# Performance work log

Hardware: AMD Instinct MI355X
Metric: run time of the kernel (lower is better)

## Reference

```python
import jax, jax.numpy as jnp
import numpy as np

H = 256       # hidden_dim
D = 64        # dim_dynamic
T = 49        # pooler_resolution**2 tokens
B = 4800      # N * nr_boxes
NP = H * D    # num_params
NOUT = H * T  # flattened output features
EPS = 1e-5


def _ln(x, g, b):
    mu = jnp.mean(x, axis=-1, keepdims=True)
    var = jnp.mean(jnp.square(x - mu), axis=-1, keepdims=True)
    return (x - mu) * jax.lax.rsqrt(var + EPS) * g + b


def setup_inputs() -> dict:
    key = jax.random.key(0)
    ks = jax.random.split(key, 12)
    s = 0.02
    inp = {
        "pro_features": jax.random.normal(ks[0], (1, B, H), jnp.float32),
        "roi_features": jax.random.normal(ks[1], (T, B, H), jnp.float32),
        # dynamic_layer: Linear(H, 2*H*D)
        "dyn_w": jax.random.normal(ks[2], (2 * NP, H), jnp.float32) * s,
        "dyn_b": jnp.zeros((2 * NP,), jnp.float32),
        "n1_g": jnp.ones((D,), jnp.float32), "n1_b": jnp.zeros((D,), jnp.float32),
        "n2_g": jnp.ones((H,), jnp.float32), "n2_b": jnp.zeros((H,), jnp.float32),
        # proj_cls1/2: Linear(H, H//8), Linear(H//8, H)
        "pc1_w": jax.random.normal(ks[3], (H // 8, H), jnp.float32) * s,
        "pc1_b": jnp.zeros((H // 8,), jnp.float32),
        "pc2_w": jax.random.normal(ks[4], (H, H // 8), jnp.float32) * s,
        "pc2_b": jnp.zeros((H,), jnp.float32),
        "n3c_g": jnp.ones((H,), jnp.float32), "n3c_b": jnp.zeros((H,), jnp.float32),
        "pr1_w": jax.random.normal(ks[5], (H // 8, H), jnp.float32) * s,
        "pr1_b": jnp.zeros((H // 8,), jnp.float32),
        "pr2_w": jax.random.normal(ks[6], (H, H // 8), jnp.float32) * s,
        "pr2_b": jnp.zeros((H,), jnp.float32),
        "n3r_g": jnp.ones((H,), jnp.float32), "n3r_b": jnp.zeros((H,), jnp.float32),
        # out_layer_cls/reg: Linear(H*T, H)
        "oc_w": jax.random.normal(ks[7], (H, NOUT), jnp.float32) * s,
        "oc_b": jnp.zeros((H,), jnp.float32),
        "n4c_g": jnp.ones((H,), jnp.float32), "n4c_b": jnp.zeros((H,), jnp.float32),
        "or_w": jax.random.normal(ks[8], (H, NOUT), jnp.float32) * s,
        "or_b": jnp.zeros((H,), jnp.float32),
        "n4r_g": jnp.ones((H,), jnp.float32), "n4r_b": jnp.zeros((H,), jnp.float32),
    }
    return inp


def reference(pro_features, roi_features, dyn_w, dyn_b, n1_g, n1_b, n2_g, n2_b,
              pc1_w, pc1_b, pc2_w, pc2_b, n3c_g, n3c_b,
              pr1_w, pr1_b, pr2_w, pr2_b, n3r_g, n3r_b,
              oc_w, oc_b, n4c_g, n4c_b, or_w, or_b, n4r_g, n4r_b):
    pro = pro_features[0]                      # (B, H)
    feats = roi_features.transpose(1, 0, 2)    # (B, T, H)
    params = pro @ dyn_w.T + dyn_b             # (B, 2*H*D)
    p1 = params[:, :NP].reshape(-1, H, D)      # (B, H, D)
    p2 = params[:, NP:].reshape(-1, D, H)      # (B, D, H)
    x = jnp.einsum('bth,bhd->btd', feats, p1)  # (B, T, D)
    x = jax.nn.relu(_ln(x, n1_g, n1_b))
    x = jnp.einsum('btd,bdh->bth', x, p2)      # (B, T, H)
    x = jax.nn.relu(_ln(x, n2_g, n2_b))
    mask_cls = jax.nn.sigmoid((pro @ pc1_w.T + pc1_b) @ pc2_w.T + pc2_b)  # (B, H)
    mask_reg = jax.nn.sigmoid((pro @ pr1_w.T + pr1_b) @ pr2_w.T + pr2_b)  # (B, H)
    fc = jax.nn.relu(_ln(x * mask_cls[:, None, :], n3c_g, n3c_b))  # (B, T, H)
    fr = jax.nn.relu(_ln(x * mask_reg[:, None, :], n3r_g, n3r_b))  # (B, T, H)
    fc = fc.reshape(fc.shape[0], -1) @ oc_w.T + oc_b               # (B, H)
    fc = jax.nn.relu(_ln(fc, n4c_g, n4c_b))
    fr = fr.reshape(fr.shape[0], -1) @ or_w.T + or_b               # (B, H)
    fr = jax.nn.relu(_ln(fr, n4r_g, n4r_b))
    return (fc, fr)
```

## Files before the change

kernel.cpp:

```cpp
#include <hip/hip_runtime.h>

#define Hc 256
#define Dc 64
#define Tc 49
#define Bc 4800
#define NPc 16384
#define KOUT 12544
#define OUTSTRIDE 1228800

typedef unsigned short u16;
typedef unsigned int u32;
typedef __bf16 bf16x8 __attribute__((ext_vector_type(8)));
typedef float f32x4 __attribute__((ext_vector_type(4)));

__device__ __forceinline__ u16 f2bf(float f){
  u32 u = __builtin_bit_cast(u32, f);
  u += 0x7fffu + ((u >> 16) & 1u);
  return (u16)(u >> 16);
}

#define GLDS16(gp, lp) __builtin_amdgcn_global_load_lds((const __attribute__((address_space(1))) void*)(gp), (__attribute__((address_space(3))) void*)(lp), 16, 0, 0)

__device__ __forceinline__ f32x4 mfma16(bf16x8 a, bf16x8 b, f32x4 c){
  return __builtin_amdgcn_mfma_f32_16x16x32_bf16(a, b, c, 0, 0, 0);
}
__device__ __forceinline__ f32x4 zero4(){ f32x4 v; v[0]=0.f; v[1]=0.f; v[2]=0.f; v[3]=0.f; return v; }

__global__ void cvt_kernel(const float* __restrict__ src, u16* __restrict__ dst, int n){
  int i = (blockIdx.x*256 + threadIdx.x)*4;
  if (i >= n) return;
  float4 v = *(const float4*)(src + i);
  u16 t[4] = {f2bf(v.x), f2bf(v.y), f2bf(v.z), f2bf(v.w)};
  *(uint2*)(dst + i) = *(const uint2*)t;
}

__global__ void procvt_kernel(const float* __restrict__ src, u16* __restrict__ dst){
  int i = (blockIdx.x*256 + threadIdx.x)*4;
  u16 t[4];
  if (i < Bc*Hc){
    float4 v = *(const float4*)(src + i);
    t[0]=f2bf(v.x); t[1]=f2bf(v.y); t[2]=f2bf(v.z); t[3]=f2bf(v.w);
  } else { t[0]=t[1]=t[2]=t[3]=0; }
  *(uint2*)(dst + i) = *(const uint2*)t;
}

__device__ __forceinline__ int dynperm(int n){
  if (n < NPc){
    int h = n >> 6, d = n & 63;
    return (d>>4)*4096 + (h>>5)*512 + ((h>>3)&3)*128 + (d&15)*8 + (h&7);
  } else {
    int m = n - NPc; int d = m >> 8, h = m & 255;
    return NPc + (h>>4)*1024 + (d>>5)*512 + ((d>>3)&3)*128 + (h&15)*8 + (d&7);
  }
}

__global__ __launch_bounds__(256) void cvt_dynw_perm(const float* __restrict__ dynw,
    const float* __restrict__ dynb, u16* __restrict__ dynwB, float* __restrict__ dynbP){
  int idx = blockIdx.x*256 + threadIdx.x;
  int n = idx >> 3, p = idx & 7;
  int pn = dynperm(n);
  const float* s = dynw + (size_t)n*256 + p*32;
  u16 t[32];
  #pragma unroll
  for (int j = 0; j < 8; j++){
    float4 v = *(const float4*)(s + j*4);
    t[j*4+0]=f2bf(v.x); t[j*4+1]=f2bf(v.y); t[j*4+2]=f2bf(v.z); t[j*4+3]=f2bf(v.w);
  }
  u16* d = dynwB + (size_t)pn*256 + p*32;
  #pragma unroll
  for (int j = 0; j < 4; j++) ((uint4*)d)[j] = ((const uint4*)t)[j];
  if (p == 0) dynbP[pn] = dynb[n];
}

__global__ __launch_bounds__(256) void masks_kernel(const float* __restrict__ pro,
    const float* __restrict__ pc1w, const float* __restrict__ pc1b,
    const float* __restrict__ pc2w, const float* __restrict__ pc2b,
    const float* __restrict__ pr1w, const float* __restrict__ pr1b,
    const float* __restrict__ pr2w, const float* __restrict__ pr2b,
    float* __restrict__ mcls, float* __restrict__ mreg)
{
  __shared__ float rowv[8][256];
  __shared__ float hv[8][33];
  const int tid = threadIdx.x;
  const int bb = blockIdx.x*8;
  #pragma unroll
  for (int q = 0; q < 8; q++) rowv[q][tid] = pro[(size_t)(bb+q)*256 + tid];
  const int bx = tid >> 5, h = tid & 31;
  __syncthreads();
  for (int br = 0; br < 2; br++){
    const float* w1 = br ? pr1w : pc1w;
    const float* b1 = br ? pr1b : pc1b;
    const float* w2 = br ? pr2w : pc2w;
    const float* b2 = br ? pr2b : pc2b;
    float* outm = br ? mreg : mcls;
    {
      float s = b1[h];
      const float* wr = w1 + h*256;
      for (int k = 0; k < 256; k += 4){
        float4 wv = *(const float4*)(wr + k);
        s += rowv[bx][k]*wv.x + rowv[bx][k+1]*wv.y + rowv[bx][k+2]*wv.z + rowv[bx][k+3]*wv.w;
      }
      hv[bx][h] = s;
    }
    __syncthreads();
    int c0 = h*8;
    float o[8];
    #pragma unroll
    for (int j = 0; j < 8; j++){
      float s2 = b2[c0+j];
      const float* w2r = w2 + (c0+j)*32;
      #pragma unroll
      for (int j2 = 0; j2 < 32; j2 += 4){
        float4 wv = *(const float4*)(w2r + j2);
        s2 += hv[bx][j2]*wv.x + hv[bx][j2+1]*wv.y + hv[bx][j2+2]*wv.z + hv[bx][j2+3]*wv.w;
      }
      o[j] = 1.f/(1.f + expf(-s2));
    }
    float* dst = outm + (size_t)(bb+bx)*256 + c0;
    *(float4*)dst = make_float4(o[0],o[1],o[2],o[3]);
    *(float4*)(dst+4) = make_float4(o[4],o[5],o[6],o[7]);
    __syncthreads();
  }
}

__global__ __launch_bounds__(512, 4) void gemm1_kernel(const u16* __restrict__ proB,
    const u16* __restrict__ dynwB, const float* __restrict__ dynbP,
    u16* __restrict__ paramsOut, int b0, int C)
{
  __shared__ u16 sm[2][2][128*64];
  const int tid = threadIdx.x;
  const int bx = blockIdx.x, by = blockIdx.y;
  const int l = tid & 63, wid = tid >> 6, l15 = l & 15, lg = l >> 4;
  const int wm = wid >> 2, wn = wid & 3;
  const char* Abase = (const char*)proB;
  const char* Bbase = (const char*)dynwB;

  auto stage = [&](int t, int buf){
    #pragma unroll
    for (int p = 0; p < 2; p++){
      int base = (wid + p*8)*1024;
      int lin = base + l*16;
      int row = lin >> 7, cb = lin & 127;
      int swz = (row & 7) << 4;
      GLDS16(Abase + (size_t)(b0 + bx*128 + row)*512 + t*128 + (cb ^ swz),
             (char*)sm[buf][0] + base);
      GLDS16(Bbase + (size_t)(by*128 + row)*512 + t*128 + (cb ^ swz),
             (char*)sm[buf][1] + base);
    }
  };

  f32x4 acc[4][2];
  #pragma unroll
  for (int i=0;i<4;i++){ acc[i][0]=zero4(); acc[i][1]=zero4(); }

  stage(0, 0);
  __syncthreads();
  for (int t = 0; t < 4; t++){
    if (t < 3) stage(t+1, (t&1)^1);
    const char* sa = (const char*)sm[t&1][0];
    const char* sb = (const char*)sm[t&1][1];
    #pragma unroll
    for (int ks = 0; ks < 2; ks++){
      bf16x8 av[4], bv[2];
      #pragma unroll
      for (int mt=0; mt<4; mt++){
        int row = wm*64 + mt*16 + l15;
        av[mt] = *(const bf16x8*)(sa + row*128 + ((ks*64 + lg*16) ^ ((row&7)<<4)));
      }
      #pragma unroll
      for (int nt=0; nt<2; nt++){
        int row = wn*32 + nt*16 + l15;
        bv[nt] = *(const bf16x8*)(sb + row*128 + ((ks*64 + lg*16) ^ ((row&7)<<4)));
      }
      #pragma unroll
      for (int mt=0; mt<4; mt++)
        #pragma unroll
        for (int nt=0; nt<2; nt++)
          acc[mt][nt] = mfma16(av[mt], bv[nt], acc[mt][nt]);
    }
    __syncthreads();
  }
  float bb[2];
  #pragma unroll
  for (int nt=0; nt<2; nt++) bb[nt] = dynbP[by*128 + wn*32 + nt*16 + l15];
  char* tile = (char*)sm;
  #pragma unroll
  for (int mt=0; mt<4; mt++)
    #pragma unroll
    for (int nt=0; nt<2; nt++)
      #pragma unroll
      for (int r=0; r<4; r++){
        int row = wm*64 + mt*16 + lg*4 + r;
        int col = wn*32 + nt*16 + l15;
        *(u16*)(tile + row*256 + ((col*2) ^ ((row&7)<<4))) = f2bf(acc[mt][nt][r] + bb[nt]);
      }
  __syncthreads();
  #pragma unroll
  for (int p = 0; p < 4; p++){
    int lin = (tid + p*512)*16;
    int row = lin >> 8, cb = lin & 255;
    int rg = bx*128 + row;
    if (rg < C){
      uint4 v = *(const uint4*)(tile + row*256 + (cb ^ ((row&7)<<4)));
      *(uint4*)((char*)paramsOut + (size_t)rg*65536 + (size_t)by*256 + cb) = v;
    }
  }
}

__global__ __launch_bounds__(256, 3) void conv_kernel(const float* __restrict__ roi,
    const u16* __restrict__ params,
    const float* __restrict__ n1g, const float* __restrict__ n1b,
    const float* __restrict__ n2g, const float* __restrict__ n2b,
    const float* __restrict__ n3cg, const float* __restrict__ n3cb,
    const float* __restrict__ n3rg, const float* __restrict__ n3rb,
    const float* __restrict__ mcls, const float* __restrict__ mreg,
    u16* __restrict__ fcin, u16* __restrict__ frin, int b0)
{
  __shared__ char lds[49152];
  const int tid = threadIdx.x, bloc = blockIdx.x, b = b0 + bloc;
  const int l = tid & 63, w = tid >> 6, l15 = l & 15, lg = l >> 4;
  const char* pbase = (const char*)params + (size_t)bloc*65536;
  const int myrow = 16*w + l15;
  const int rrow = tid >> 2, rk4 = tid & 3;
  const float* rsrc = roi + ((size_t)rrow*Bc + b)*256 + rk4*32;

  float4 rva[8];
  if (rrow < Tc){
    #pragma unroll
    for (int j = 0; j < 8; j++) rva[j] = *(const float4*)(rsrc + j*4);
  }
  #pragma unroll
  for (int p = 0; p < 4; p++)
    GLDS16(pbase + p*8192 + tid*16, lds + 16384 + p*4096 + w*1024);

  float* SCf = (float*)(lds + 40960);
  {
    float mc = mcls[(size_t)b*256+tid], mr = mreg[(size_t)b*256+tid];
    float g2 = n2g[tid], b2v = n2b[tid];
    SCf[0*256+tid] = g2*mc; SCf[1*256+tid] = b2v*mc;
    SCf[2*256+tid] = n3cg[tid]; SCf[3*256+tid] = n3cb[tid];
    SCf[4*256+tid] = g2*mr; SCf[5*256+tid] = b2v*mr;
    SCf[6*256+tid] = n3rg[tid]; SCf[7*256+tid] = n3rb[tid];
  }

  auto wfeats = [&](const float4* rv){
    u16 tt[32];
    if (rrow < Tc){
      #pragma unroll
      for (int j = 0; j < 8; j++){
        float4 v = rv[j];
        tt[j*4+0]=f2bf(v.x); tt[j*4+1]=f2bf(v.y); tt[j*4+2]=f2bf(v.z); tt[j*4+3]=f2bf(v.w);
      }
    } else {
      #pragma unroll
      for (int j=0;j<32;j++) tt[j]=0;
    }
    int swz = (rrow & 7) << 4;
    #pragma unroll
    for (int c2 = 0; c2 < 4; c2++)
      *(uint4*)(lds + rrow*256 + ((rk4*64 + c2*16) ^ swz)) = ((const uint4*)tt)[c2];
  };
  wfeats(rva);
  float4 rvb[8];
  if (rrow < Tc){
    #pragma unroll
    for (int j = 0; j < 8; j++) rvb[j] = *(const float4*)(rsrc + 128 + j*4);
  }
  __syncthreads();

  f32x4 xacc[4];
  #pragma unroll
  for (int i=0;i<4;i++) xacc[i] = zero4();
  #pragma unroll
  for (int ks = 0; ks < 4; ks++){
    bf16x8 af = *(const bf16x8*)(lds + myrow*256 + ((ks*64 + lg*16) ^ ((myrow&7)<<4)));
    #pragma unroll
    for (int nt = 0; nt < 4; nt++){
      bf16x8 bf = *(const bf16x8*)(lds + 16384 + nt*4096 + ks*1024 + lg*256 + l15*16);
      xacc[nt] = mfma16(af, bf, xacc[nt]);
    }
  }
  __syncthreads();
  #pragma unroll
  for (int p = 0; p < 4; p++)
    GLDS16(pbase + p*8192 + 4096 + tid*16, lds + 16384 + p*4096 + w*1024);
  wfeats(rvb);
  __syncthreads();
  #pragma unroll
  for (int ks = 0; ks < 4; ks++){
    bf16x8 af = *(const bf16x8*)(lds + myrow*256 + ((ks*64 + lg*16) ^ ((myrow&7)<<4)));
    #pragma unroll
    for (int nt = 0; nt < 4; nt++){
      bf16x8 bf = *(const bf16x8*)(lds + 16384 + nt*4096 + ks*1024 + lg*256 + l15*16);
      xacc[nt] = mfma16(af, bf, xacc[nt]);
    }
  }
  __syncthreads();

  #pragma unroll
  for (int p = 0; p < 8; p++)
    GLDS16(pbase + 32768 + p*4096 + tid*16, lds + p*4096 + w*1024);
  {
    float g1v[4], b1v[4];
    #pragma unroll
    for (int nt=0; nt<4; nt++){ g1v[nt] = n1g[nt*16+l15]; b1v[nt] = n1b[nt*16+l15]; }
    #pragma unroll
    for (int r = 0; r < 4; r++){
      float s = xacc[0][r]+xacc[1][r]+xacc[2][r]+xacc[3][r];
      float q = xacc[0][r]*xacc[0][r]+xacc[1][r]*xacc[1][r]
              + xacc[2][r]*xacc[2][r]+xacc[3][r]*xacc[3][r];
      #pragma unroll
      for (int m = 1; m < 16; m <<= 1){ s += __shfl_xor(s, m); q += __shfl_xor(q, m); }
      float mu = s*(1.f/64.f);
      float rs = rsqrtf(q*(1.f/64.f) - mu*mu + 1e-5f);
      int row = 16*w + lg*4 + r;
      int swz = (row & 7) << 4;
      #pragma unroll
      for (int nt=0; nt<4; nt++){
        float yv = fmaxf((xacc[nt][r]-mu)*rs*g1v[nt] + b1v[nt], 0.f);
        *(u16*)(lds + 32768 + row*128 + ((2*(nt*16+l15)) ^ swz)) = f2bf(yv);
      }
    }
  }
  __syncthreads();

  f32x4 acc[16];
  #pragma unroll
  for (int i=0;i<16;i++) acc[i] = zero4();
  #pragma unroll
  for (int ks = 0; ks < 2; ks++){
    bf16x8 ay = *(const bf16x8*)(lds + 32768 + myrow*128 + ((ks*64 + lg*16) ^ ((myrow&7)<<4)));
    #pragma unroll
    for (int nt = 0; nt < 16; nt++){
      bf16x8 bp = *(const bf16x8*)(lds + nt*2048 + ks*1024 + lg*256 + l15*16);
      acc[nt] = mfma16(ay, bp, acc[nt]);
    }
  }

  #pragma unroll
  for (int r = 0; r < 4; r++){
    float s = 0.f, q = 0.f;
    #pragma unroll
    for (int nt=0; nt<16; nt++){ float v = acc[nt][r]; s += v; q += v*v; }
    #pragma unroll
    for (int m = 1; m < 16; m <<= 1){ s += __shfl_xor(s, m); q += __shfl_xor(q, m); }
    float mu = s*(1.f/256.f);
    float rs = rsqrtf(q*(1.f/256.f) - mu*mu + 1e-5f);
    #pragma unroll
    for (int nt=0; nt<16; nt++) acc[nt][r] = (acc[nt][r]-mu)*rs;
  }
  __syncthreads();

  float* SCf2 = (float*)(lds + 40960);
  for (int br = 0; br < 2; br++){
    float s3[4] = {0.f,0.f,0.f,0.f}, q3[4] = {0.f,0.f,0.f,0.f};
    #pragma unroll
    for (int nt=0; nt<16; nt++){
      int col = nt*16 + l15;
      float gm = SCf2[(4*br)*256 + col], bm = SCf2[(4*br+1)*256 + col];
      #pragma unroll
      for (int r=0; r<4; r++){
        float u = fmaxf(acc[nt][r]*gm + bm, 0.f);
        s3[r] += u; q3[r] += u*u;
      }
    }
    float m3[4], r3[4];
    #pragma unroll
    for (int r=0; r<4; r++){
      float s = s3[r], q = q3[r];
      #pragma unroll
      for (int m = 1; m < 16; m <<= 1){ s += __shfl_xor(s, m); q += __shfl_xor(q, m); }
      float mu = s*(1.f/256.f);
      m3[r] = mu; r3[r] = rsqrtf(q*(1.f/256.f) - mu*mu + 1e-5f);
    }
    #pragma unroll
    for (int nt=0; nt<16; nt++){
      int col = nt*16 + l15;
      float gm = SCf2[(4*br)*256 + col], bm = SCf2[(4*br+1)*256 + col];
      float g3 = SCf2[(4*br+2)*256 + col], b3 = SCf2[(4*br+3)*256 + col];
      #pragma unroll
      for (int r=0; r<4; r++){
        int row = 16*w + lg*4 + r;
        float u = fmaxf(acc[nt][r]*gm + bm, 0.f);
        float f = fmaxf((u - m3[r])*r3[r]*g3 + b3, 0.f);
        *(u16*)(lds + row*512 + ((2*col) ^ ((row&7)<<4))) = f2bf(f);
      }
    }
    {
      u16* outp = (br ? frin : fcin) + (size_t)b * KOUT;
      #pragma unroll
      for (int p = 0; p < 8; p++){
        int off = w*8192 + p*1024 + l*16;
        int row = off >> 9;
        if (row < Tc){
          int cb = off & 511;
          uint4 v = *(const uint4*)(lds + row*512 + (cb ^ ((row&7)<<4)));
          *(uint4*)((char*)outp + off) = v;
        }
      }
    }
  }
}

__global__ __launch_bounds__(256, 4) void outgemm_part(
    const u16* __restrict__ fcin, const u16* __restrict__ frin,
    const u16* __restrict__ ocw, const u16* __restrict__ orw,
    float* __restrict__ pbuf)
{
  __shared__ u16 smA[64*64];
  __shared__ u16 smB[256*64];
  const int tid = threadIdx.x;
  const int z = blockIdx.y, sp = blockIdx.z;
  const int m0 = blockIdx.x * 64;
  const u16* A = z ? frin : fcin;
  const u16* W = z ? orw : ocw;
  const int l = tid & 63, w = tid >> 6, l15 = l & 15, lg = l >> 4;

  f32x4 acc[4][4];
  #pragma unroll
  for (int i=0;i<4;i++)
    #pragma unroll
    for (int j=0;j<4;j++) acc[i][j] = zero4();

  const int kt0 = (sp*49) >> 1, kt1 = ((sp+1)*49) >> 1;
  for (int kt = kt0; kt < kt1; kt++){
    #pragma unroll
    for (int p = 0; p < 2; p++){
      int base = (w + p*4)*1024;
      int lin = base + l*16;
      int row = lin >> 7, cb = lin & 127;
      GLDS16((const char*)A + (size_t)(m0 + row)*25088 + kt*128 + (cb ^ ((row & 7) << 4)), (char*)smA + base);
    }
    #pragma unroll
    for (int p = 0; p < 8; p++){
      int base = (w + p*4)*1024;
      int lin = base + l*16;
      int n = lin >> 7, cb = lin & 127;
      GLDS16((const char*)W + (size_t)n*25088 + kt*128 + (cb ^ ((n & 7) << 4)), (char*)smB + base);
    }
    __syncthreads();
    #pragma unroll
    for (int ks = 0; ks < 2; ks++){
      bf16x8 av[4], bv[4];
      #pragma unroll
      for (int mt=0; mt<4; mt++){
        int row = mt*16 + l15;
        av[mt] = *(const bf16x8*)((const char*)smA + row*128 + ((ks*64 + lg*16) ^ ((row&7)<<4)));
      }
      #pragma unroll
      for (int nt=0; nt<4; nt++){
        int row = w*64 + nt*16 + l15;
        bv[nt] = *(const bf16x8*)((const char*)smB + row*128 + ((ks*64 + lg*16) ^ ((row&7)<<4)));
      }
      #pragma unroll
      for (int mt=0; mt<4; mt++)
        #pragma unroll
        for (int nt=0; nt<4; nt++)
          acc[mt][nt] = mfma16(av[mt], bv[nt], acc[mt][nt]);
    }
    __syncthreads();
  }
  float* pb = pbuf + ((size_t)(z*8 + sp)*Bc)*256;
  #pragma unroll
  for (int mt=0; mt<4; mt++)
    #pragma unroll
    for (int r=0; r<4; r++){
      int row = m0 + mt*16 + lg*4 + r;
      #pragma unroll
      for (int nt=0; nt<4; nt++)
        pb[(size_t)row*256 + w*64 + nt*16 + l15] = acc[mt][nt][r];
    }
}

__global__ __launch_bounds__(256) void ln4fin(const float* __restrict__ pbuf,
    const float* __restrict__ ocb, const float* __restrict__ orb,
    const float* __restrict__ n4cg, const float* __restrict__ n4cb,
    const float* __restrict__ n4rg, const float* __restrict__ n4rb,
    float* __restrict__ dout)
{
  int R = blockIdx.x*4 + (threadIdx.x >> 6);
  int z = R >= Bc;
  int box = R - z*Bc;
  int lane = threadIdx.x & 63;
  int col = lane*4;
  float4 v = make_float4(0.f,0.f,0.f,0.f);
  #pragma unroll
  for (int s = 0; s < 8; s++){
    float4 p = *(const float4*)(pbuf + ((size_t)(z*8 + s)*Bc + box)*256 + col);
    v.x += p.x; v.y += p.y; v.z += p.z; v.w += p.w;
  }
  float4 bi = *(const float4*)((z ? orb : ocb) + col);
  v.x += bi.x; v.y += bi.y; v.z += bi.z; v.w += bi.w;
  float s = v.x+v.y+v.z+v.w;
  float q = v.x*v.x+v.y*v.y+v.z*v.z+v.w*v.w;
  #pragma unroll
  for (int m = 1; m < 64; m <<= 1){ s += __shfl_xor(s, m); q += __shfl_xor(q, m); }
  float mu = s*(1.f/256.f);
  float rs = rsqrtf(q*(1.f/256.f) - mu*mu + 1e-5f);
  float4 g = *(const float4*)((z ? n4rg : n4cg) + col);
  float4 bb = *(const float4*)((z ? n4rb : n4cb) + col);
  float4 o;
  o.x = fmaxf((v.x-mu)*rs*g.x + bb.x, 0.f);
  o.y = fmaxf((v.y-mu)*rs*g.y + bb.y, 0.f);
  o.z = fmaxf((v.z-mu)*rs*g.z + bb.z, 0.f);
  o.w = fmaxf((v.w-mu)*rs*g.w + bb.w, 0.f);
  *(float4*)(dout + (size_t)z*OUTSTRIDE + (size_t)box*256 + col) = o;
}

extern "C" void kernel_launch(void* const* d_in, const int* in_sizes, int n_in,
                              void* d_out, int out_size, void* d_ws, size_t ws_size,
                              hipStream_t stream)
{
  (void)in_sizes; (void)n_in; (void)out_size;
  const float* pro  = (const float*)d_in[0];
  const float* roi  = (const float*)d_in[1];
  const float* dynw = (const float*)d_in[2];
  const float* dynb = (const float*)d_in[3];
  const float* n1g = (const float*)d_in[4];
  const float* n1b = (const float*)d_in[5];
  const float* n2g = (const float*)d_in[6];
  const float* n2b = (const float*)d_in[7];
  const float* pc1w = (const float*)d_in[8];
  const float* pc1b = (const float*)d_in[9];
  const float* pc2w = (const float*)d_in[10];
  const float* pc2b = (const float*)d_in[11];
  const float* n3cg = (const float*)d_in[12];
  const float* n3cb = (const float*)d_in[13];
  const float* pr1w = (const float*)d_in[14];
  const float* pr1b = (const float*)d_in[15];
  const float* pr2w = (const float*)d_in[16];
  const float* pr2b = (const float*)d_in[17];
  const float* n3rg = (const float*)d_in[18];
  const float* n3rb = (const float*)d_in[19];
  const float* ocw = (const float*)d_in[20];
  const float* ocb = (const float*)d_in[21];
  const float* n4cg = (const float*)d_in[22];
  const float* n4cb = (const float*)d_in[23];
  const float* orw = (const float*)d_in[24];
  const float* orb = (const float*)d_in[25];
  const float* n4rg = (const float*)d_in[26];
  const float* n4rb = (const float*)d_in[27];
  float* dout = (float*)d_out;

  char* ws = (char*)d_ws;
  size_t off = 0;
  auto alloc = [&](size_t bytes) -> char* {
    char* p = ws + off;
    off += (bytes + 255) & ~(size_t)255;
    return p;
  };
  u16* dynwB = (u16*)alloc((size_t)32768*256*2);
  float* dynbP = (float*)alloc((size_t)32768*4);
  u16* ocwB  = (u16*)alloc((size_t)12544*256*2);
  u16* orwB  = (u16*)alloc((size_t)12544*256*2);
  u16* proB  = (u16*)alloc((size_t)4864*256*2);
  float* mcls = (float*)alloc((size_t)4800*256*4);
  float* mreg = (float*)alloc((size_t)4800*256*4);
  u16* fcinF  = (u16*)alloc((size_t)Bc*25088);
  u16* frinF  = (u16*)alloc((size_t)Bc*25088);
  float* pbufF = (float*)alloc((size_t)16*Bc*256*4);
  size_t fixedOff = off;

  int C = 480;
  const int copts[] = {1200, 960, 800, 600, 480};
  for (int i = 0; i < (int)(sizeof(copts)/sizeof(int)); i++){
    size_t need = fixedOff + (size_t)copts[i]*65536;
    if (need <= ws_size){ C = copts[i]; break; }
  }
  u16* paramsC = (u16*)alloc((size_t)C*65536);

  cvt_dynw_perm<<<1024, 256, 0, stream>>>(dynw, dynb, dynwB, dynbP);
  cvt_kernel<<<3136, 256, 0, stream>>>(ocw, ocwB, 12544*256);
  cvt_kernel<<<3136, 256, 0, stream>>>(orw, orwB, 12544*256);
  procvt_kernel<<<1216, 256, 0, stream>>>(pro, proB);
  masks_kernel<<<600, 256, 0, stream>>>(pro, pc1w, pc1b, pc2w, pc2b,
                                        pr1w, pr1b, pr2w, pr2b, mcls, mreg);
  int nch = (Bc + C - 1) / C;
  for (int c = 0; c < nch; c++){
    int b0 = c*C;
    int Cc = (b0 + C <= Bc) ? C : (Bc - b0);
    gemm1_kernel<<<dim3((Cc+127)/128, 256), 512, 0, stream>>>(proB, dynwB, dynbP, paramsC, b0, Cc);
    conv_kernel<<<Cc, 256, 0, stream>>>(roi, paramsC, n1g, n1b, n2g, n2b,
                                        n3cg, n3cb, n3rg, n3rb, mcls, mreg,
                                        fcinF, frinF, b0);
  }
  outgemm_part<<<dim3(75, 2, 8), 256, 0, stream>>>(fcinF, frinF, ocwB, orwB, pbufF);
  ln4fin<<<2400, 256, 0, stream>>>(pbufF, ocb, orb, n4cg, n4cb, n4rg, n4rb, dout);
}
```

Baseline: 872.8 us.

## Load GEMM operands directly from global into registers with double buffering

The conv kernel now reads roi features and dynamic params straight from global memory into MFMA operand registers, converting to bf16 in-register. It double-buffers these loads and drops most LDS staging and barriers, which also shrinks LDS to 40 KB. The output GEMM likewise replaces LDS tiling with direct per-lane global loads using register ping-pong, and its occupancy hint changes from 4 to 3. The pro bf16 buffer is padded larger. The aim is to remove LDS traffic and sync overhead, at the cost of uncoalesced strided global reads and no cross-wave reuse through LDS.

```diff
diff --git a/kernel.cpp b/kernel.cpp
--- a/kernel.cpp
+++ b/kernel.cpp
@@ -216,24 +216,16 @@
     const float* __restrict__ mcls, const float* __restrict__ mreg,
     u16* __restrict__ fcin, u16* __restrict__ frin, int b0)
 {
-  __shared__ char lds[49152];
+  __shared__ char lds[40960];
   const int tid = threadIdx.x, bloc = blockIdx.x, b = b0 + bloc;
   const int l = tid & 63, w = tid >> 6, l15 = l & 15, lg = l >> 4;
   const char* pbase = (const char*)params + (size_t)bloc*65536;
-  const int myrow = 16*w + l15;
-  const int rrow = tid >> 2, rk4 = tid & 3;
-  const float* rsrc = roi + ((size_t)rrow*Bc + b)*256 + rk4*32;
-
-  float4 rva[8];
-  if (rrow < Tc){
-    #pragma unroll
-    for (int j = 0; j < 8; j++) rva[j] = *(const float4*)(rsrc + j*4);
-  }
-  #pragma unroll
-  for (int p = 0; p < 4; p++)
-    GLDS16(pbase + p*8192 + tid*16, lds + 16384 + p*4096 + w*1024);
-
-  float* SCf = (float*)(lds + 40960);
+  const int wbase = w*8192;
+  const int arow = 16*w + l15;
+  const int crow = (arow < Tc) ? arow : (Tc-1);
+  const float* asrc = roi + ((size_t)crow*Bc + b)*256 + lg*8;
+
+  float* SCf = (float*)(lds + 32768);
   {
     float mc = mcls[(size_t)b*256+tid], mr = mreg[(size_t)b*256+tid];
     float g2 = n2g[tid], b2v = n2b[tid];
@@ -243,63 +235,41 @@
     SCf[6*256+tid] = n3rg[tid]; SCf[7*256+tid] = n3rb[tid];
   }
 
-  auto wfeats = [&](const float4* rv){
-    u16 tt[32];
-    if (rrow < Tc){
-      #pragma unroll
-      for (int j = 0; j < 8; j++){
-        float4 v = rv[j];
-        tt[j*4+0]=f2bf(v.x); tt[j*4+1]=f2bf(v.y); tt[j*4+2]=f2bf(v.z); tt[j*4+3]=f2bf(v.w);
-      }
+  const char* p1a = pbase + lg*256 + l15*16;
+  f32x4 xacc[4];
+  #pragma unroll
+  for (int i=0;i<4;i++) xacc[i] = zero4();
+
+  f32x4 aA0, aA1, aB0, aB1;
+  bf16x8 bA[4], bB[4];
+  aA0 = *(const f32x4*)(asrc);  aA1 = *(const f32x4*)(asrc + 4);
+  #pragma unroll
+  for (int nt=0; nt<4; nt++) bA[nt] = *(const bf16x8*)(p1a + nt*8192);
+  #pragma unroll
+  for (int kk = 0; kk < 8; kk++){
+    if (kk & 1){
+      if (kk < 7){
+        aA0 = *(const f32x4*)(asrc + (kk+1)*32); aA1 = *(const f32x4*)(asrc + (kk+1)*32 + 4);
+        #pragma unroll
+        for (int nt=0; nt<4; nt++) bA[nt] = *(const bf16x8*)(p1a + nt*8192 + (kk+1)*1024);
+      }
+      bf16x8 af;
+      #pragma unroll
+      for (int j=0;j<4;j++){ af[j] = (__bf16)aB0[j]; af[4+j] = (__bf16)aB1[j]; }
+      #pragma unroll
+      for (int nt=0; nt<4; nt++) xacc[nt] = mfma16(af, bB[nt], xacc[nt]);
     } else {
-      #pragma unroll
-      for (int j=0;j<32;j++) tt[j]=0;
-    }
-    int swz = (rrow & 7) << 4;
-    #pragma unroll
-    for (int c2 = 0; c2 < 4; c2++)
-      *(uint4*)(lds + rrow*256 + ((rk4*64 + c2*16) ^ swz)) = ((const uint4*)tt)[c2];
-  };
-  wfeats(rva);
-  float4 rvb[8];
-  if (rrow < Tc){
-    #pragma unroll
-    for (int j = 0; j < 8; j++) rvb[j] = *(const float4*)(rsrc + 128 + j*4);
-  }
-  __syncthreads();
-
-  f32x4 xacc[4];
-  #pragma unroll
-  for (int i=0;i<4;i++) xacc[i] = zero4();
-  #pragma unroll
-  for (int ks = 0; ks < 4; ks++){
-    bf16x8 af = *(const bf16x8*)(lds + myrow*256 + ((ks*64 + lg*16) ^ ((myrow&7)<<4)));
-    #pragma unroll
-    for (int nt = 0; nt < 4; nt++){
-      bf16x8 bf = *(const bf16x8*)(lds + 16384 + nt*4096 + ks*1024 + lg*256 + l15*16);
-      xacc[nt] = mfma16(af, bf, xacc[nt]);
-    }
-  }
-  __syncthreads();
-  #pragma unroll
-  for (int p = 0; p < 4; p++)
-    GLDS16(pbase + p*8192 + 4096 + tid*16, lds + 16384 + p*4096 + w*1024);
-  wfeats(rvb);
-  __syncthreads();
-  #pragma unroll
-  for (int ks = 0; ks < 4; ks++){
-    bf16x8 af = *(const bf16x8*)(lds + myrow*256 + ((ks*64 + lg*16) ^ ((myrow&7)<<4)));
-    #pragma unroll
-    for (int nt = 0; nt < 4; nt++){
-      bf16x8 bf = *(const bf16x8*)(lds + 16384 + nt*4096 + ks*1024 + lg*256 + l15*16);
-      xacc[nt] = mfma16(af, bf, xacc[nt]);
-    }
-  }
-  __syncthreads();
-
-  #pragma unroll
-  for (int p = 0; p < 8; p++)
-    GLDS16(pbase + 32768 + p*4096 + tid*16, lds + p*4096 + w*1024);
+      aB0 = *(const f32x4*)(asrc + (kk+1)*32); aB1 = *(const f32x4*)(asrc + (kk+1)*32 + 4);
+      #pragma unroll
+      for (int nt=0; nt<4; nt++) bB[nt] = *(const bf16x8*)(p1a + nt*8192 + (kk+1)*1024);
+      bf16x8 af;
+      #pragma unroll
+      for (int j=0;j<4;j++){ af[j] = (__bf16)aA0[j]; af[4+j] = (__bf16)aA1[j]; }
+      #pragma unroll
+      for (int nt=0; nt<4; nt++) xacc[nt] = mfma16(af, bA[nt], xacc[nt]);
+    }
+  }
+
   {
     float g1v[4], b1v[4];
     #pragma unroll
@@ -313,27 +283,45 @@
       for (int m = 1; m < 16; m <<= 1){ s += __shfl_xor(s, m); q += __shfl_xor(q, m); }
       float mu = s*(1.f/64.f);
       float rs = rsqrtf(q*(1.f/64.f) - mu*mu + 1e-5f);
-      int row = 16*w + lg*4 + r;
-      int swz = (row & 7) << 4;
+      int lr = lg*4 + r;
+      int swz = (lr & 7) << 4;
       #pragma unroll
       for (int nt=0; nt<4; nt++){
         float yv = fmaxf((xacc[nt][r]-mu)*rs*g1v[nt] + b1v[nt], 0.f);
-        *(u16*)(lds + 32768 + row*128 + ((2*(nt*16+l15)) ^ swz)) = f2bf(yv);
-      }
-    }
-  }
-  __syncthreads();
-
+        *(u16*)(lds + wbase + lr*128 + ((2*(nt*16+l15)) ^ swz)) = f2bf(yv);
+      }
+    }
+  }
+
+  bf16x8 ay[2];
+  #pragma unroll
+  for (int ks=0; ks<2; ks++)
+    ay[ks] = *(const bf16x8*)(lds + wbase + l15*128 + ((ks*64 + lg*16) ^ ((l15&7)<<4)));
+
+  const char* p2a = pbase + 32768 + lg*256 + l15*16;
   f32x4 acc[16];
   #pragma unroll
   for (int i=0;i<16;i++) acc[i] = zero4();
-  #pragma unroll
-  for (int ks = 0; ks < 2; ks++){
-    bf16x8 ay = *(const bf16x8*)(lds + 32768 + myrow*128 + ((ks*64 + lg*16) ^ ((myrow&7)<<4)));
-    #pragma unroll
-    for (int nt = 0; nt < 16; nt++){
-      bf16x8 bp = *(const bf16x8*)(lds + nt*2048 + ks*1024 + lg*256 + l15*16);
-      acc[nt] = mfma16(ay, bp, acc[nt]);
+  bf16x8 pA[4], pB[4];
+  #pragma unroll
+  for (int nt2=0; nt2<4; nt2++) pA[nt2] = *(const bf16x8*)(p2a + nt2*2048);
+  #pragma unroll
+  for (int idx = 0; idx < 8; idx++){
+    int ks = idx >> 2, g = idx & 3;
+    if (idx & 1){
+      if (idx < 7){
+        int ks2 = (idx+1)>>2, g2 = (idx+1)&3;
+        #pragma unroll
+        for (int nt2=0; nt2<4; nt2++) pA[nt2] = *(const bf16x8*)(p2a + (g2*4+nt2)*2048 + ks2*1024);
+      }
+      #pragma unroll
+      for (int nt2=0; nt2<4; nt2++) acc[g*4+nt2] = mfma16(ay[ks], pB[nt2], acc[g*4+nt2]);
+    } else {
+      int ks2 = (idx+1)>>2, g2 = (idx+1)&3;
+      #pragma unroll
+      for (int nt2=0; nt2<4; nt2++) pB[nt2] = *(const bf16x8*)(p2a + (g2*4+nt2)*2048 + ks2*1024);
+      #pragma unroll
+      for (int nt2=0; nt2<4; nt2++) acc[g*4+nt2] = mfma16(ay[ks], pA[nt2], acc[g*4+nt2]);
     }
   }
 
@@ -349,15 +337,15 @@
     #pragma unroll
     for (int nt=0; nt<16; nt++) acc[nt][r] = (acc[nt][r]-mu)*rs;
   }
+
   __syncthreads();
 
-  float* SCf2 = (float*)(lds + 40960);
   for (int br = 0; br < 2; br++){
     float s3[4] = {0.f,0.f,0.f,0.f}, q3[4] = {0.f,0.f,0.f,0.f};
     #pragma unroll
     for (int nt=0; nt<16; nt++){
       int col = nt*16 + l15;
-      float gm = SCf2[(4*br)*256 + col], bm = SCf2[(4*br+1)*256 + col];
+      float gm = SCf[(4*br)*256 + col], bm = SCf[(4*br+1)*256 + col];
       #pragma unroll
       for (int r=0; r<4; r++){
         float u = fmaxf(acc[nt][r]*gm + bm, 0.f);
@@ -376,8 +364,8 @@
     #pragma unroll
     for (int nt=0; nt<16; nt++){
       int col = nt*16 + l15;
-      float gm = SCf2[(4*br)*256 + col], bm = SCf2[(4*br+1)*256 + col];
-      float g3 = SCf2[(4*br+2)*256 + col], b3 = SCf2[(4*br+3)*256 + col];
+      float gm = SCf[(4*br)*256 + col], bm = SCf[(4*br+1)*256 + col];
+      float g3 = SCf[(4*br+2)*256 + col], b3 = SCf[(4*br+3)*256 + col];
       #pragma unroll
       for (int r=0; r<4; r++){
         int row = 16*w + lg*4 + r;
@@ -402,13 +390,11 @@
   }
 }
 
-__global__ __launch_bounds__(256, 4) void outgemm_part(
+__global__ __launch_bounds__(256, 3) void outgemm_part(
     const u16* __restrict__ fcin, const u16* __restrict__ frin,
     const u16* __restrict__ ocw, const u16* __restrict__ orw,
     float* __restrict__ pbuf)
 {
-  __shared__ u16 smA[64*64];
-  __shared__ u16 smB[256*64];
   const int tid = threadIdx.x;
   const int z = blockIdx.y, sp = blockIdx.z;
   const int m0 = blockIdx.x * 64;
@@ -416,50 +402,57 @@
   const u16* W = z ? orw : ocw;
   const int l = tid & 63, w = tid >> 6, l15 = l & 15, lg = l >> 4;
 
+  const char* Abase = (const char*)A + (size_t)(m0 + l15)*25088 + lg*16;
+  const char* Bbase = (const char*)W + (size_t)(w*64 + l15)*25088 + lg*16;
+
   f32x4 acc[4][4];
   #pragma unroll
   for (int i=0;i<4;i++)
     #pragma unroll
     for (int j=0;j<4;j++) acc[i][j] = zero4();
 
-  const int kt0 = (sp*49) >> 1, kt1 = ((sp+1)*49) >> 1;
-  for (int kt = kt0; kt < kt1; kt++){
-    #pragma unroll
-    for (int p = 0; p < 2; p++){
-      int base = (w + p*4)*1024;
-      int lin = base + l*16;
-      int row = lin >> 7, cb = lin & 127;
-      GLDS16((const char*)A + (size_t)(m0 + row)*25088 + kt*128 + (cb ^ ((row & 7) << 4)), (char*)smA + base);
-    }
-    #pragma unroll
-    for (int p = 0; p < 8; p++){
-      int base = (w + p*4)*1024;
-      int lin = base + l*16;
-      int n = lin >> 7, cb = lin & 127;
-      GLDS16((const char*)W + (size_t)n*25088 + kt*128 + (cb ^ ((n & 7) << 4)), (char*)smB + base);
-    }
-    __syncthreads();
-    #pragma unroll
-    for (int ks = 0; ks < 2; ks++){
-      bf16x8 av[4], bv[4];
-      #pragma unroll
-      for (int mt=0; mt<4; mt++){
-        int row = mt*16 + l15;
-        av[mt] = *(const bf16x8*)((const char*)smA + row*128 + ((ks*64 + lg*16) ^ ((row&7)<<4)));
-      }
-      #pragma unroll
-      for (int nt=0; nt<4; nt++){
-        int row = w*64 + nt*16 + l15;
-        bv[nt] = *(const bf16x8*)((const char*)smB + row*128 + ((ks*64 + lg*16) ^ ((row&7)<<4)));
-      }
-      #pragma unroll
-      for (int mt=0; mt<4; mt++)
-        #pragma unroll
-        for (int nt=0; nt<4; nt++)
-          acc[mt][nt] = mfma16(av[mt], bv[nt], acc[mt][nt]);
-    }
-    __syncthreads();
-  }
+  const int kt0 = (sp*49) >> 1;
+  const int npair = (((sp+1)*49) >> 1) - kt0;
+  const int N = npair*2;
+
+  bf16x8 avA[4], bvA[4], avB[4], bvB[4];
+  {
+    int off = kt0*128;
+    #pragma unroll
+    for (int mt=0; mt<4; mt++) avA[mt] = *(const bf16x8*)(Abase + (size_t)mt*16*25088 + off);
+    #pragma unroll
+    for (int nt=0; nt<4; nt++) bvA[nt] = *(const bf16x8*)(Bbase + (size_t)nt*16*25088 + off);
+  }
+  for (int p = 0; p < npair; p++){
+    int base = p*2;
+    {
+      int idx = base + 1;
+      int off = (kt0 + (idx>>1))*128 + (idx&1)*64;
+      #pragma unroll
+      for (int mt=0; mt<4; mt++) avB[mt] = *(const bf16x8*)(Abase + (size_t)mt*16*25088 + off);
+      #pragma unroll
+      for (int nt=0; nt<4; nt++) bvB[nt] = *(const bf16x8*)(Bbase + (size_t)nt*16*25088 + off);
+    }
+    #pragma unroll
+    for (int mt=0; mt<4; mt++)
+      #pragma unroll
+      for (int nt=0; nt<4; nt++)
+        acc[mt][nt] = mfma16(avA[mt], bvA[nt], acc[mt][nt]);
+    if (base + 2 < N){
+      int idx = base + 2;
+      int off = (kt0 + (idx>>1))*128 + (idx&1)*64;
+      #pragma unroll
+      for (int mt=0; mt<4; mt++) avA[mt] = *(const bf16x8*)(Abase + (size_t)mt*16*25088 + off);
+      #pragma unroll
+      for (int nt=0; nt<4; nt++) bvA[nt] = *(const bf16x8*)(Bbase + (size_t)nt*16*25088 + off);
+    }
+    #pragma unroll
+    for (int mt=0; mt<4; mt++)
+      #pragma unroll
+      for (int nt=0; nt<4; nt++)
+        acc[mt][nt] = mfma16(avB[mt], bvB[nt], acc[mt][nt]);
+  }
+
   float* pb = pbuf + ((size_t)(z*8 + sp)*Bc)*256;
   #pragma unroll
   for (int mt=0; mt<4; mt++)
@@ -553,7 +546,7 @@
   float* dynbP = (float*)alloc((size_t)32768*4);
   u16* ocwB  = (u16*)alloc((size_t)12544*256*2);
   u16* orwB  = (u16*)alloc((size_t)12544*256*2);
-  u16* proB  = (u16*)alloc((size_t)4864*256*2);
+  u16* proB  = (u16*)alloc((size_t)4992*256*2);
   float* mcls = (float*)alloc((size_t)4800*256*4);
   float* mreg = (float*)alloc((size_t)4800*256*4);
   u16* fcinF  = (u16*)alloc((size_t)Bc*25088);
@@ -572,7 +565,7 @@
   cvt_dynw_perm<<<1024, 256, 0, stream>>>(dynw, dynb, dynwB, dynbP);
   cvt_kernel<<<3136, 256, 0, stream>>>(ocw, ocwB, 12544*256);
   cvt_kernel<<<3136, 256, 0, stream>>>(orw, orwB, 12544*256);
-  procvt_kernel<<<1216, 256, 0, stream>>>(pro, proB);
+  procvt_kernel<<<1248, 256, 0, stream>>>(pro, proB);
   masks_kernel<<<600, 256, 0, stream>>>(pro, pc1w, pc1b, pc2w, pc2b,
                                         pr1w, pr1b, pr2w, pr2b, mcls, mreg);
   int nch = (Bc + C - 1) / C;
```

New measurement: 973.1 us. 11.5% more time.
